# Performance work log

Hardware: AMD Instinct MI355X
Metric: run time of the kernel (lower is better)

Reference implementation:

```python
import jax, jax.numpy as jnp
import numpy as np

N = 50000    # nodes
E = 800000   # edges
D = 128      # emb_dim
L = 3        # num_layers
NA = 9       # atom feature columns
AV = 64      # atom vocab per column
NB = 3       # bond feature columns
BV = 8       # bond vocab per column
BN_EPS = 1e-5


def setup_inputs() -> dict:
    key = jax.random.key(0)
    ks = jax.random.split(key, 12)
    s = 0.05
    x = jax.random.randint(ks[0], (N, NA), 0, AV)
    edge_attr = jax.random.randint(ks[1], (E, NB), 0, BV)
    src = jax.random.randint(ks[2], (E,), 0, N)
    dst = jax.random.randint(ks[3], (E,), 0, N)
    atom_emb = jax.random.normal(ks[4], (NA, AV, D), jnp.float32) * s
    bond_emb = jax.random.normal(ks[5], (L, NB, BV, D), jnp.float32) * s  # one BondEncoder per layer
    W1 = jax.random.normal(ks[6], (L, D, D), jnp.float32) * s
    b1 = jnp.zeros((L, D), jnp.float32)
    W2 = jax.random.normal(ks[7], (L, D, D), jnp.float32) * s
    b2 = jnp.zeros((L, D), jnp.float32)
    g1 = jnp.ones((L, D), jnp.float32)   # mlp-internal BN gamma
    be1 = jnp.zeros((L, D), jnp.float32)  # mlp-internal BN beta
    og = jnp.ones((L, D), jnp.float32)   # outer BN gamma
    ob = jnp.zeros((L, D), jnp.float32)  # outer BN beta
    gin_eps = jnp.zeros((L,), jnp.float32)
    return {"x": x, "edge_attr": edge_attr, "src": src, "dst": dst,
            "atom_emb": atom_emb, "bond_emb": bond_emb,
            "W1": W1, "b1": b1, "g1": g1, "be1": be1,
            "W2": W2, "b2": b2, "gin_eps": gin_eps, "og": og, "ob": ob}


def _bn(h, gamma, beta):
    # BatchNorm1d, training-mode (batch statistics, biased var)
    mu = jnp.mean(h, axis=0)
    var = jnp.mean(jnp.square(h - mu), axis=0)
    return gamma * (h - mu) * jax.lax.rsqrt(var + BN_EPS) + beta


def _multi_embed(tables, idx):
    # tables: [C, V, D], idx: [n, C] -> sum_c tables[c, idx[:, c]]  -> [n, D]
    return tables[jnp.arange(tables.shape[0])[None, :], idx].sum(axis=1)


def reference(x, edge_attr, src, dst, atom_emb, bond_emb,
              W1, b1, g1, be1, W2, b2, gin_eps, og, ob):
    h = _multi_embed(atom_emb, x)  # AtomEncoder: [N, D]
    for l in range(L):
        ee = _multi_embed(bond_emb[l], edge_attr)          # BondEncoder: [E, D]
        m = jax.nn.relu(h[src] + ee)                       # gather + combine
        agg = jax.ops.segment_sum(m, dst, num_segments=N)  # scatter-sum to dst
        z = (1.0 + gin_eps[l]) * h + agg
        z = z @ W1[l] + b1[l]
        z = jax.nn.relu(_bn(z, g1[l], be1[l]))
        z = z @ W2[l] + b2[l]
        h2 = _bn(z, og[l], ob[l])                          # outer BatchNorm
        if l < L - 1:
            h2 = jax.nn.relu(h2)                           # dropout is no-op (eval)
        h = h2
    return h  # JK='last'
```

## Files before the change

### kernel.cpp

```cpp
#include <hip/hip_runtime.h>

#define N_NODES 50000
#define N_EDGES 800000
#define DIM     128
#define D4      32
#define NLAYERS 3
#define NATOM   9
#define AVOC    64
#define NBOND   3
#define BVOC    8
#define BN_EPS  1e-5f
#define INVN    (1.0f / (float)N_NODES)

__global__ __launch_bounds__(256) void atom_kernel(
    const int* __restrict__ x, const float* __restrict__ ae,
    float* __restrict__ h, int n_nodes)
{
    int tid  = threadIdx.x;
    int lane = tid & 31;
    int node = blockIdx.x * 8 + (tid >> 5);
    if (node >= n_nodes) return;
    const int* xr = x + node * NATOM;
    const float4* ae4 = (const float4*)ae;
    float4 acc = make_float4(0.f, 0.f, 0.f, 0.f);
#pragma unroll
    for (int c = 0; c < NATOM; c++) {
        int v = xr[c];
        float4 t = ae4[(c * AVOC + v) * D4 + lane];
        acc.x += t.x; acc.y += t.y; acc.z += t.z; acc.w += t.w;
    }
    ((float4*)h)[node * D4 + lane] = acc;
}

__global__ void hist_kernel(const int* __restrict__ dst, int* __restrict__ counts, int n)
{
    int e = blockIdx.x * blockDim.x + threadIdx.x;
    if (e < n) atomicAdd(&counts[dst[e]], 1);
}

__global__ __launch_bounds__(256) void scan1_kernel(
    const int* __restrict__ counts, int* __restrict__ incl,
    int* __restrict__ blk_sums, int n)
{
    __shared__ int sh[256];
    int tid = threadIdx.x;
    int i = blockIdx.x * 256 + tid;
    int v = (i < n) ? counts[i] : 0;
    sh[tid] = v;
    __syncthreads();
    for (int off = 1; off < 256; off <<= 1) {
        int t = (tid >= off) ? sh[tid - off] : 0;
        __syncthreads();
        sh[tid] += t;
        __syncthreads();
    }
    if (i < n) incl[i] = sh[tid];
    if (tid == 255) blk_sums[blockIdx.x] = sh[255];
}

__global__ __launch_bounds__(256) void scan2_kernel(int* __restrict__ blk_sums, int nblk)
{
    __shared__ int sh[256];
    int tid = threadIdx.x;
    int v = (tid < nblk) ? blk_sums[tid] : 0;
    sh[tid] = v;
    __syncthreads();
    for (int off = 1; off < 256; off <<= 1) {
        int t = (tid >= off) ? sh[tid - off] : 0;
        __syncthreads();
        sh[tid] += t;
        __syncthreads();
    }
    if (tid < nblk) blk_sums[tid] = sh[tid] - v;
}

__global__ __launch_bounds__(256) void scan3_kernel(
    const int* __restrict__ counts, const int* __restrict__ incl,
    const int* __restrict__ blk_sums, int* __restrict__ row_ptr,
    int* __restrict__ cursor, int n)
{
    int i = blockIdx.x * 256 + threadIdx.x;
    if (i >= n) return;
    int total = incl[i] + blk_sums[blockIdx.x];
    row_ptr[i + 1] = total;
    cursor[i] = total - counts[i];
    if (i == 0) row_ptr[0] = 0;
}

__global__ void fill_kernel(const int* __restrict__ dst, const int* __restrict__ src,
                            const int* __restrict__ edge_attr, int* __restrict__ cursor,
                            int* __restrict__ esrc, int* __restrict__ ebond, int n)
{
    int e = blockIdx.x * blockDim.x + threadIdx.x;
    if (e >= n) return;
    int p = atomicAdd(&cursor[dst[e]], 1);
    esrc[p] = src[e];
    const int* ea = edge_attr + e * 3;
    ebond[p] = ea[0] | (ea[1] << 8) | (ea[2] << 16);
}

template <bool BNIN>
__global__ __launch_bounds__(256) void agg_kernel(
    const float* __restrict__ zin, const int* __restrict__ row_ptr,
    const int* __restrict__ esrc, const int* __restrict__ ebond,
    const float* __restrict__ bond_l, const float* __restrict__ epsp,
    const float* __restrict__ sum2p, const float* __restrict__ ssq2p,
    const float* __restrict__ gam, const float* __restrict__ bet,
    float* __restrict__ z, int n_nodes)
{
    __shared__ float4 bt[NBOND * BVOC * D4];
    int tid = threadIdx.x;
    const float4* b4 = (const float4*)bond_l;
    for (int i = tid; i < NBOND * BVOC * D4; i += 256) bt[i] = b4[i];
    __syncthreads();

    int lane = tid & 31;
    int node = blockIdx.x * 8 + (tid >> 5);
    if (node >= n_nodes) return;

    float4 sc = make_float4(1.f, 1.f, 1.f, 1.f);
    float4 sf = make_float4(0.f, 0.f, 0.f, 0.f);
    if (BNIN) {
        float4 sm = ((const float4*)sum2p)[lane];
        float4 sq = ((const float4*)ssq2p)[lane];
        float4 g  = ((const float4*)gam)[lane];
        float4 b  = ((const float4*)bet)[lane];
        float mux = sm.x * INVN, muy = sm.y * INVN, muz = sm.z * INVN, muw = sm.w * INVN;
        float vx = fmaxf(sq.x * INVN - mux * mux, 0.f);
        float vy = fmaxf(sq.y * INVN - muy * muy, 0.f);
        float vz = fmaxf(sq.z * INVN - muz * muz, 0.f);
        float vw = fmaxf(sq.w * INVN - muw * muw, 0.f);
        sc.x = g.x * rsqrtf(vx + BN_EPS); sc.y = g.y * rsqrtf(vy + BN_EPS);
        sc.z = g.z * rsqrtf(vz + BN_EPS); sc.w = g.w * rsqrtf(vw + BN_EPS);
        sf.x = fmaf(-mux, sc.x, b.x); sf.y = fmaf(-muy, sc.y, b.y);
        sf.z = fmaf(-muz, sc.z, b.z); sf.w = fmaf(-muw, sc.w, b.w);
    }

    float eps = epsp[0];
    int j0 = row_ptr[node], j1 = row_ptr[node + 1];
    const float4* zin4 = (const float4*)zin;
    float4 acc = make_float4(0.f, 0.f, 0.f, 0.f);

#define HEFF(v) do { if (BNIN) { \
        (v).x = fmaxf(fmaf((v).x, sc.x, sf.x), 0.f); \
        (v).y = fmaxf(fmaf((v).y, sc.y, sf.y), 0.f); \
        (v).z = fmaxf(fmaf((v).z, sc.z, sf.z), 0.f); \
        (v).w = fmaxf(fmaf((v).w, sc.w, sf.w), 0.f); } } while (0)

    int j = j0;
    for (; j + 2 <= j1; j += 2) {
        int s0 = esrc[j],     bb0 = ebond[j];
        int s1 = esrc[j + 1], bb1 = ebond[j + 1];
        float4 h0 = zin4[(size_t)s0 * D4 + lane];
        float4 h1 = zin4[(size_t)s1 * D4 + lane];
        float4 a0 = bt[(bb0 & 255) * D4 + lane];
        float4 a1 = bt[(BVOC + ((bb0 >> 8) & 255)) * D4 + lane];
        float4 a2 = bt[(2 * BVOC + ((bb0 >> 16) & 255)) * D4 + lane];
        float4 c0 = bt[(bb1 & 255) * D4 + lane];
        float4 c1 = bt[(BVOC + ((bb1 >> 8) & 255)) * D4 + lane];
        float4 c2 = bt[(2 * BVOC + ((bb1 >> 16) & 255)) * D4 + lane];
        HEFF(h0); HEFF(h1);
        acc.x += fmaxf(h0.x + a0.x + a1.x + a2.x, 0.f) + fmaxf(h1.x + c0.x + c1.x + c2.x, 0.f);
        acc.y += fmaxf(h0.y + a0.y + a1.y + a2.y, 0.f) + fmaxf(h1.y + c0.y + c1.y + c2.y, 0.f);
        acc.z += fmaxf(h0.z + a0.z + a1.z + a2.z, 0.f) + fmaxf(h1.z + c0.z + c1.z + c2.z, 0.f);
        acc.w += fmaxf(h0.w + a0.w + a1.w + a2.w, 0.f) + fmaxf(h1.w + c0.w + c1.w + c2.w, 0.f);
    }
    if (j < j1) {
        int s0 = esrc[j], bb0 = ebond[j];
        float4 h0 = zin4[(size_t)s0 * D4 + lane];
        float4 a0 = bt[(bb0 & 255) * D4 + lane];
        float4 a1 = bt[(BVOC + ((bb0 >> 8) & 255)) * D4 + lane];
        float4 a2 = bt[(2 * BVOC + ((bb0 >> 16) & 255)) * D4 + lane];
        HEFF(h0);
        acc.x += fmaxf(h0.x + a0.x + a1.x + a2.x, 0.f);
        acc.y += fmaxf(h0.y + a0.y + a1.y + a2.y, 0.f);
        acc.z += fmaxf(h0.z + a0.z + a1.z + a2.z, 0.f);
        acc.w += fmaxf(h0.w + a0.w + a1.w + a2.w, 0.f);
    }

    float4 hn = zin4[(size_t)node * D4 + lane];
    HEFF(hn);
#undef HEFF
    float s1v = 1.f + eps;
    float4 o;
    o.x = fmaf(s1v, hn.x, acc.x);
    o.y = fmaf(s1v, hn.y, acc.y);
    o.z = fmaf(s1v, hn.z, acc.z);
    o.w = fmaf(s1v, hn.w, acc.w);
    ((float4*)z)[(size_t)node * D4 + lane] = o;
}

template <bool BN>
__global__ __launch_bounds__(512, 4) void gemm_kernel(
    const float* __restrict__ A, const float* __restrict__ W,
    const float* __restrict__ bias,
    const float* __restrict__ sum_in, const float* __restrict__ ssq_in,
    const float* __restrict__ gam, const float* __restrict__ bet,
    float* __restrict__ sum_out, float* __restrict__ ssq_out,
    float* __restrict__ out, int nrows)
{
    __shared__ float Bs[DIM * DIM];
    __shared__ float scs[DIM], shs[DIM];
    int tid = threadIdx.x;
    {
        float4* Bs4 = (float4*)Bs;
        const float4* W4 = (const float4*)W;
        for (int i = tid; i < DIM * D4; i += 512) Bs4[i] = W4[i];
        if (BN && tid < DIM) {
            float mu = sum_in[tid] * INVN;
            float var = fmaxf(ssq_in[tid] * INVN - mu * mu, 0.f);
            float sc = gam[tid] * rsqrtf(var + BN_EPS);
            scs[tid] = sc;
            shs[tid] = fmaf(-mu, sc, bet[tid]);
        }
    }
    __syncthreads();

    int tx = tid & 31;
    int ty = tid >> 5;
    int row0 = blockIdx.x * 128 + ty * 8;

    int ar[8];
#pragma unroll
    for (int r = 0; r < 8; r++) {
        int rr = row0 + r; if (rr > nrows - 1) rr = nrows - 1;
        ar[r] = rr * D4;
    }

    float4 acc[8];
#pragma unroll
    for (int r = 0; r < 8; r++) acc[r] = make_float4(0.f, 0.f, 0.f, 0.f);

    const float4* A4 = (const float4*)A;
    const float4* Bs4 = (const float4*)Bs;
    const float4* sc4p = (const float4*)scs;
    const float4* sh4p = (const float4*)shs;

    for (int k = 0; k < DIM; k += 4) {
        float4 b0 = Bs4[(k + 0) * D4 + tx];
        float4 b1 = Bs4[(k + 1) * D4 + tx];
        float4 b2 = Bs4[(k + 2) * D4 + tx];
        float4 b3 = Bs4[(k + 3) * D4 + tx];
        float4 sc, sf;
        if (BN) { sc = sc4p[k >> 2]; sf = sh4p[k >> 2]; }
#pragma unroll
        for (int r = 0; r < 8; r++) {
            float4 a = A4[ar[r] + (k >> 2)];
            if (BN) {
                a.x = fmaxf(fmaf(a.x, sc.x, sf.x), 0.f);
                a.y = fmaxf(fmaf(a.y, sc.y, sf.y), 0.f);
                a.z = fmaxf(fmaf(a.z, sc.z, sf.z), 0.f);
                a.w = fmaxf(fmaf(a.w, sc.w, sf.w), 0.f);
            }
            acc[r].x = fmaf(a.w, b3.x, fmaf(a.z, b2.x, fmaf(a.y, b1.x, fmaf(a.x, b0.x, acc[r].x))));
            acc[r].y = fmaf(a.w, b3.y, fmaf(a.z, b2.y, fmaf(a.y, b1.y, fmaf(a.x, b0.y, acc[r].y))));
            acc[r].z = fmaf(a.w, b3.z, fmaf(a.z, b2.z, fmaf(a.y, b1.z, fmaf(a.x, b0.z, acc[r].z))));
            acc[r].w = fmaf(a.w, b3.w, fmaf(a.z, b2.w, fmaf(a.y, b1.w, fmaf(a.x, b0.w, acc[r].w))));
        }
    }

    float4 bv = ((const float4*)bias)[tx];
    float4* out4 = (float4*)out;
    float4 s4 = make_float4(0.f, 0.f, 0.f, 0.f);
    float4 q4 = make_float4(0.f, 0.f, 0.f, 0.f);
#pragma unroll
    for (int r = 0; r < 8; r++) {
        int row = row0 + r;
        if (row < nrows) {
            float4 o;
            o.x = acc[r].x + bv.x; o.y = acc[r].y + bv.y;
            o.z = acc[r].z + bv.z; o.w = acc[r].w + bv.w;
            out4[(size_t)row * D4 + tx] = o;
            s4.x += o.x; s4.y += o.y; s4.z += o.z; s4.w += o.w;
            q4.x = fmaf(o.x, o.x, q4.x); q4.y = fmaf(o.y, o.y, q4.y);
            q4.z = fmaf(o.z, o.z, q4.z); q4.w = fmaf(o.w, o.w, q4.w);
        }
    }

    __syncthreads();
    float4* red = (float4*)Bs;
    red[tid] = s4;
    red[512 + tid] = q4;
    __syncthreads();
#pragma unroll
    for (int off = 256; off >= 32; off >>= 1) {
        if (tid < off) {
            float4 a = red[tid], b = red[tid + off];
            a.x += b.x; a.y += b.y; a.z += b.z; a.w += b.w;
            red[tid] = a;
            float4 c = red[512 + tid], d = red[512 + tid + off];
            c.x += d.x; c.y += d.y; c.z += d.z; c.w += d.w;
            red[512 + tid] = c;
        }
        __syncthreads();
    }
    if (tid < 32) {
        float4 s = red[tid], q = red[512 + tid];
        atomicAdd(&sum_out[tid * 4 + 0], s.x);
        atomicAdd(&sum_out[tid * 4 + 1], s.y);
        atomicAdd(&sum_out[tid * 4 + 2], s.z);
        atomicAdd(&sum_out[tid * 4 + 3], s.w);
        atomicAdd(&ssq_out[tid * 4 + 0], q.x);
        atomicAdd(&ssq_out[tid * 4 + 1], q.y);
        atomicAdd(&ssq_out[tid * 4 + 2], q.z);
        atomicAdd(&ssq_out[tid * 4 + 3], q.w);
    }
}

__global__ __launch_bounds__(256) void apply_final_kernel(
    const float* __restrict__ X, const float* __restrict__ sum2,
    const float* __restrict__ ssq2, const float* __restrict__ gam,
    const float* __restrict__ bet, float* __restrict__ out, int n4)
{
    int i = blockIdx.x * blockDim.x + threadIdx.x;
    if (i >= n4) return;
    int c4 = i & 31;
    float4 sm = ((const float4*)sum2)[c4];
    float4 sq = ((const float4*)ssq2)[c4];
    float4 g  = ((const float4*)gam)[c4];
    float4 b  = ((const float4*)bet)[c4];
    float mux = sm.x * INVN, muy = sm.y * INVN, muz = sm.z * INVN, muw = sm.w * INVN;
    float4 sc, sf;
    sc.x = g.x * rsqrtf(fmaxf(sq.x * INVN - mux * mux, 0.f) + BN_EPS);
    sc.y = g.y * rsqrtf(fmaxf(sq.y * INVN - muy * muy, 0.f) + BN_EPS);
    sc.z = g.z * rsqrtf(fmaxf(sq.z * INVN - muz * muz, 0.f) + BN_EPS);
    sc.w = g.w * rsqrtf(fmaxf(sq.w * INVN - muw * muw, 0.f) + BN_EPS);
    sf.x = fmaf(-mux, sc.x, b.x); sf.y = fmaf(-muy, sc.y, b.y);
    sf.z = fmaf(-muz, sc.z, b.z); sf.w = fmaf(-muw, sc.w, b.w);
    float4 v = ((const float4*)X)[i];
    v.x = fmaf(v.x, sc.x, sf.x);
    v.y = fmaf(v.y, sc.y, sf.y);
    v.z = fmaf(v.z, sc.z, sf.z);
    v.w = fmaf(v.w, sc.w, sf.w);
    ((float4*)out)[i] = v;
}

extern "C" void kernel_launch(void* const* d_in, const int* in_sizes, int n_in,
                              void* d_out, int out_size, void* d_ws, size_t ws_size,
                              hipStream_t stream)
{
    const int*   x         = (const int*)d_in[0];
    const int*   edge_attr = (const int*)d_in[1];
    const int*   src       = (const int*)d_in[2];
    const int*   dst       = (const int*)d_in[3];
    const float* atom_emb  = (const float*)d_in[4];
    const float* bond_emb  = (const float*)d_in[5];
    const float* W1        = (const float*)d_in[6];
    const float* b1        = (const float*)d_in[7];
    const float* g1        = (const float*)d_in[8];
    const float* be1       = (const float*)d_in[9];
    const float* W2        = (const float*)d_in[10];
    const float* b2        = (const float*)d_in[11];
    const float* gin_eps   = (const float*)d_in[12];
    const float* og        = (const float*)d_in[13];
    const float* ob        = (const float*)d_in[14];
    float* out = (float*)d_out;

    const size_t ND = (size_t)N_NODES * DIM;
    const int NBLK = (N_NODES + 255) / 256;

    float* stats = (float*)d_ws;
    float* zagg  = stats + 2048;
    float* z2buf = zagg + ND;
    float* z1    = out;
    int* counts   = (int*)(z2buf + ND);
    int* row_ptr  = counts + N_NODES;
    int* cursor   = row_ptr + N_NODES + 1;
    int* esrc     = cursor + N_NODES;
    int* ebond    = esrc + N_EDGES;
    int* incl     = ebond + N_EDGES;
    int* blk_sums = incl + N_NODES;

    hipMemsetAsync(counts, 0, N_NODES * sizeof(int), stream);
    hipMemsetAsync(stats, 0, 1536 * sizeof(float), stream);
    atom_kernel<<<(N_NODES + 7) / 8, 256, 0, stream>>>(x, atom_emb, z2buf, N_NODES);
    hist_kernel<<<(N_EDGES + 255) / 256, 256, 0, stream>>>(dst, counts, N_EDGES);
    scan1_kernel<<<NBLK, 256, 0, stream>>>(counts, incl, blk_sums, N_NODES);
    scan2_kernel<<<1, 256, 0, stream>>>(blk_sums, NBLK);
    scan3_kernel<<<NBLK, 256, 0, stream>>>(counts, incl, blk_sums, row_ptr, cursor, N_NODES);
    fill_kernel<<<(N_EDGES + 255) / 256, 256, 0, stream>>>(dst, src, edge_attr, cursor,
                                                           esrc, ebond, N_EDGES);

    for (int l = 0; l < NLAYERS; l++) {
        const float* bond_l = bond_emb + (size_t)l * NBOND * BVOC * DIM;
        float* st   = stats + (size_t)l * 512;
        float* sum1 = st,       *ssq1 = st + 128;
        float* sum2 = st + 256, *ssq2 = st + 384;

        if (l == 0) {
            agg_kernel<false><<<(N_NODES + 7) / 8, 256, 0, stream>>>(
                z2buf, row_ptr, esrc, ebond, bond_l, gin_eps + l,
                nullptr, nullptr, nullptr, nullptr, zagg, N_NODES);
        } else {
            float* stp = stats + (size_t)(l - 1) * 512;
            agg_kernel<true><<<(N_NODES + 7) / 8, 256, 0, stream>>>(
                z2buf, row_ptr, esrc, ebond, bond_l, gin_eps + l,
                stp + 256, stp + 384, og + (l - 1) * DIM, ob + (l - 1) * DIM,
                zagg, N_NODES);
        }
        gemm_kernel<false><<<(N_NODES + 127) / 128, 512, 0, stream>>>(
            zagg, W1 + (size_t)l * DIM * DIM, b1 + l * DIM,
            nullptr, nullptr, nullptr, nullptr, sum1, ssq1, z1, N_NODES);
        gemm_kernel<true><<<(N_NODES + 127) / 128, 512, 0, stream>>>(
            z1, W2 + (size_t)l * DIM * DIM, b2 + l * DIM,
            sum1, ssq1, g1 + l * DIM, be1 + l * DIM, sum2, ssq2, z2buf, N_NODES);
    }
    {
        float* stp = stats + (size_t)(NLAYERS - 1) * 512;
        apply_final_kernel<<<((int)(N_NODES * D4) + 255) / 256, 256, 0, stream>>>(
            z2buf, stp + 256, stp + 384, og + (NLAYERS - 1) * DIM,
            ob + (NLAYERS - 1) * DIM, out, N_NODES * D4);
    }
}
```

Before: 792.1 us.

## Shrink GEMM blocks to 32 rows and stage weights in two 64-row halves

The node GEMM kernel now uses 256-thread blocks covering 32 rows (4 rows per thread) instead of 512 threads over 128 rows. The weight matrix is staged into shared memory in two 64-row halves, halving LDS use per block. The aim is more resident blocks per CU and many more blocks in the grid for better load balance. In exchange, each block reloads all of W per 32 rows, there are extra barriers per K-half, and about four times as many atomic adds go to the BN statistics.

```diff
diff --git a/kernel.cpp b/kernel.cpp
--- a/kernel.cpp
+++ b/kernel.cpp
@@ -190,8 +190,9 @@
     ((float4*)z)[(size_t)node * D4 + lane] = o;
 }
 
+#define GROWS 32
 template <bool BN>
-__global__ __launch_bounds__(512, 4) void gemm_kernel(
+__global__ __launch_bounds__(256, 4) void gemm_kernel(
     const float* __restrict__ A, const float* __restrict__ W,
     const float* __restrict__ bias,
     const float* __restrict__ sum_in, const float* __restrict__ ssq_in,
@@ -199,63 +200,65 @@
     float* __restrict__ sum_out, float* __restrict__ ssq_out,
     float* __restrict__ out, int nrows)
 {
-    __shared__ float Bs[DIM * DIM];
+    __shared__ float Ws[64 * DIM];
     __shared__ float scs[DIM], shs[DIM];
     int tid = threadIdx.x;
-    {
-        float4* Bs4 = (float4*)Bs;
-        const float4* W4 = (const float4*)W;
-        for (int i = tid; i < DIM * D4; i += 512) Bs4[i] = W4[i];
-        if (BN && tid < DIM) {
-            float mu = sum_in[tid] * INVN;
-            float var = fmaxf(ssq_in[tid] * INVN - mu * mu, 0.f);
-            float sc = gam[tid] * rsqrtf(var + BN_EPS);
-            scs[tid] = sc;
-            shs[tid] = fmaf(-mu, sc, bet[tid]);
-        }
-    }
-    __syncthreads();
+    if (BN && tid < DIM) {
+        float mu = sum_in[tid] * INVN;
+        float var = fmaxf(ssq_in[tid] * INVN - mu * mu, 0.f);
+        float sc = gam[tid] * rsqrtf(var + BN_EPS);
+        scs[tid] = sc;
+        shs[tid] = fmaf(-mu, sc, bet[tid]);
+    }
 
     int tx = tid & 31;
     int ty = tid >> 5;
-    int row0 = blockIdx.x * 128 + ty * 8;
-
-    int ar[8];
-#pragma unroll
-    for (int r = 0; r < 8; r++) {
+    int row0 = blockIdx.x * GROWS + ty * 4;
+
+    int ar[4];
+#pragma unroll
+    for (int r = 0; r < 4; r++) {
         int rr = row0 + r; if (rr > nrows - 1) rr = nrows - 1;
         ar[r] = rr * D4;
     }
 
-    float4 acc[8];
-#pragma unroll
-    for (int r = 0; r < 8; r++) acc[r] = make_float4(0.f, 0.f, 0.f, 0.f);
-
-    const float4* A4 = (const float4*)A;
-    const float4* Bs4 = (const float4*)Bs;
+    float4 acc[4];
+#pragma unroll
+    for (int r = 0; r < 4; r++) acc[r] = make_float4(0.f, 0.f, 0.f, 0.f);
+
+    const float4* A4  = (const float4*)A;
+    const float4* W4  = (const float4*)W;
+    const float4* Ws4 = (const float4*)Ws;
+    float4* WsS = (float4*)Ws;
     const float4* sc4p = (const float4*)scs;
     const float4* sh4p = (const float4*)shs;
 
-    for (int k = 0; k < DIM; k += 4) {
-        float4 b0 = Bs4[(k + 0) * D4 + tx];
-        float4 b1 = Bs4[(k + 1) * D4 + tx];
-        float4 b2 = Bs4[(k + 2) * D4 + tx];
-        float4 b3 = Bs4[(k + 3) * D4 + tx];
-        float4 sc, sf;
-        if (BN) { sc = sc4p[k >> 2]; sf = sh4p[k >> 2]; }
-#pragma unroll
-        for (int r = 0; r < 8; r++) {
-            float4 a = A4[ar[r] + (k >> 2)];
-            if (BN) {
-                a.x = fmaxf(fmaf(a.x, sc.x, sf.x), 0.f);
-                a.y = fmaxf(fmaf(a.y, sc.y, sf.y), 0.f);
-                a.z = fmaxf(fmaf(a.z, sc.z, sf.z), 0.f);
-                a.w = fmaxf(fmaf(a.w, sc.w, sf.w), 0.f);
+    for (int p = 0; p < 2; ++p) {
+        int kb = p * 64;
+        __syncthreads();
+        for (int i = tid; i < 64 * D4; i += 256) WsS[i] = W4[kb * D4 + i];
+        __syncthreads();
+        for (int k = 0; k < 64; k += 4) {
+            float4 b0 = Ws4[(k + 0) * D4 + tx];
+            float4 b1 = Ws4[(k + 1) * D4 + tx];
+            float4 b2 = Ws4[(k + 2) * D4 + tx];
+            float4 b3 = Ws4[(k + 3) * D4 + tx];
+            float4 sc, sf;
+            if (BN) { sc = sc4p[(kb + k) >> 2]; sf = sh4p[(kb + k) >> 2]; }
+#pragma unroll
+            for (int r = 0; r < 4; r++) {
+                float4 a = A4[ar[r] + ((kb + k) >> 2)];
+                if (BN) {
+                    a.x = fmaxf(fmaf(a.x, sc.x, sf.x), 0.f);
+                    a.y = fmaxf(fmaf(a.y, sc.y, sf.y), 0.f);
+                    a.z = fmaxf(fmaf(a.z, sc.z, sf.z), 0.f);
+                    a.w = fmaxf(fmaf(a.w, sc.w, sf.w), 0.f);
+                }
+                acc[r].x = fmaf(a.w, b3.x, fmaf(a.z, b2.x, fmaf(a.y, b1.x, fmaf(a.x, b0.x, acc[r].x))));
+                acc[r].y = fmaf(a.w, b3.y, fmaf(a.z, b2.y, fmaf(a.y, b1.y, fmaf(a.x, b0.y, acc[r].y))));
+                acc[r].z = fmaf(a.w, b3.z, fmaf(a.z, b2.z, fmaf(a.y, b1.z, fmaf(a.x, b0.z, acc[r].z))));
+                acc[r].w = fmaf(a.w, b3.w, fmaf(a.z, b2.w, fmaf(a.y, b1.w, fmaf(a.x, b0.w, acc[r].w))));
             }
-            acc[r].x = fmaf(a.w, b3.x, fmaf(a.z, b2.x, fmaf(a.y, b1.x, fmaf(a.x, b0.x, acc[r].x))));
-            acc[r].y = fmaf(a.w, b3.y, fmaf(a.z, b2.y, fmaf(a.y, b1.y, fmaf(a.x, b0.y, acc[r].y))));
-            acc[r].z = fmaf(a.w, b3.z, fmaf(a.z, b2.z, fmaf(a.y, b1.z, fmaf(a.x, b0.z, acc[r].z))));
-            acc[r].w = fmaf(a.w, b3.w, fmaf(a.z, b2.w, fmaf(a.y, b1.w, fmaf(a.x, b0.w, acc[r].w))));
         }
     }
 
@@ -264,7 +267,7 @@
     float4 s4 = make_float4(0.f, 0.f, 0.f, 0.f);
     float4 q4 = make_float4(0.f, 0.f, 0.f, 0.f);
 #pragma unroll
-    for (int r = 0; r < 8; r++) {
+    for (int r = 0; r < 4; r++) {
         int row = row0 + r;
         if (row < nrows) {
             float4 o;
@@ -278,24 +281,24 @@
     }
 
     __syncthreads();
-    float4* red = (float4*)Bs;
+    float4* red = (float4*)Ws;
     red[tid] = s4;
-    red[512 + tid] = q4;
+    red[256 + tid] = q4;
     __syncthreads();
 #pragma unroll
-    for (int off = 256; off >= 32; off >>= 1) {
+    for (int off = 128; off >= 32; off >>= 1) {
         if (tid < off) {
             float4 a = red[tid], b = red[tid + off];
             a.x += b.x; a.y += b.y; a.z += b.z; a.w += b.w;
             red[tid] = a;
-            float4 c = red[512 + tid], d = red[512 + tid + off];
+            float4 c = red[256 + tid], d = red[256 + tid + off];
             c.x += d.x; c.y += d.y; c.z += d.z; c.w += d.w;
-            red[512 + tid] = c;
+            red[256 + tid] = c;
         }
         __syncthreads();
     }
     if (tid < 32) {
-        float4 s = red[tid], q = red[512 + tid];
+        float4 s = red[tid], q = red[256 + tid];
         atomicAdd(&sum_out[tid * 4 + 0], s.x);
         atomicAdd(&sum_out[tid * 4 + 1], s.y);
         atomicAdd(&sum_out[tid * 4 + 2], s.z);
@@ -381,6 +384,7 @@
     fill_kernel<<<(N_EDGES + 255) / 256, 256, 0, stream>>>(dst, src, edge_attr, cursor,
                                                            esrc, ebond, N_EDGES);
 
+    const int GGRID = (N_NODES + GROWS - 1) / GROWS;
     for (int l = 0; l < NLAYERS; l++) {
         const float* bond_l = bond_emb + (size_t)l * NBOND * BVOC * DIM;
         float* st   = stats + (size_t)l * 512;
@@ -398,10 +402,10 @@
                 stp + 256, stp + 384, og + (l - 1) * DIM, ob + (l - 1) * DIM,
                 zagg, N_NODES);
         }
-        gemm_kernel<false><<<(N_NODES + 127) / 128, 512, 0, stream>>>(
+        gemm_kernel<false><<<GGRID, 256, 0, stream>>>(
             zagg, W1 + (size_t)l * DIM * DIM, b1 + l * DIM,
             nullptr, nullptr, nullptr, nullptr, sum1, ssq1, z1, N_NODES);
-        gemm_kernel<true><<<(N_NODES + 127) / 128, 512, 0, stream>>>(
+        gemm_kernel<true><<<GGRID, 256, 0, stream>>>(
             z1, W2 + (size_t)l * DIM * DIM, b2 + l * DIM,
             sum1, ssq1, g1 + l * DIM, be1 + l * DIM, sum2, ssq2, z2buf, N_NODES);
     }
```

After: 1.419 ms. 79.1% more time.
